# Kernel tuning notes

Measured on AMD Instinct MI355X. Metric: run time of the kernel, lower is better.

## Reference

```python
import jax, jax.numpy as jnp
import numpy as np

D = 128      # feature dim
H = 8        # heads
DH = D // H  # dim per head
N = 100000   # nodes
E = 600000   # edges
BN_EPS = 1e-5


def _bn(x, g, b, m, v):
    # BatchNorm1d in eval mode (running stats)
    return (x - m) * jax.lax.rsqrt(v + BN_EPS) * g + b


def setup_inputs() -> dict:
    key = jax.random.key(0)
    ks = jax.random.split(key, 32)
    s = 1.0 / np.sqrt(D)
    inp = {
        "x": jax.random.normal(ks[0], (N, D), jnp.float32),
        "edge_index": jax.random.randint(ks[1], (2, E), 0, N, jnp.int64),
        # type embeddings (1 node type, 1 edge type)
        "nt_emb": jax.random.normal(ks[2], (1, D), jnp.float32),
        "et_emb": jax.random.normal(ks[3], (1, D), jnp.float32),
        # merge_node_edge_attr: Linear(2D,D) -> BN -> ReLU -> Linear(D,D)
        "mW1": jax.random.normal(ks[4], (2 * D, D), jnp.float32) * s,
        "mb1": jnp.zeros((D,), jnp.float32),
        "m_g": jnp.ones((D,), jnp.float32),
        "m_b": jnp.zeros((D,), jnp.float32),
        "m_m": jax.random.normal(ks[5], (D,), jnp.float32) * 0.1,
        "m_v": jax.random.uniform(ks[6], (D,), jnp.float32, 0.5, 1.5),
        "mW2": jax.random.normal(ks[7], (D, D), jnp.float32) * s,
        "mb2": jnp.zeros((D,), jnp.float32),
        # residual projection (no bias)
        "resW": jax.random.normal(ks[8], (D, D), jnp.float32) * s,
        # attention projections
        "qW": jax.random.normal(ks[9], (D, D), jnp.float32) * s,
        "qb": jnp.zeros((D,), jnp.float32),
        "kW": jax.random.normal(ks[10], (D, D), jnp.float32) * s,
        "kb": jnp.zeros((D,), jnp.float32),
        "vW": jax.random.normal(ks[11], (D, D), jnp.float32) * s,
        "vb": jnp.zeros((D,), jnp.float32),
        # output mlp: Linear -> BN -> LeakyReLU -> Linear
        "oW1": jax.random.normal(ks[12], (D, D), jnp.float32) * s,
        "ob1": jnp.zeros((D,), jnp.float32),
        "o_g": jnp.ones((D,), jnp.float32),
        "o_b": jnp.zeros((D,), jnp.float32),
        "o_m": jax.random.normal(ks[13], (D,), jnp.float32) * 0.1,
        "o_v": jax.random.uniform(ks[14], (D,), jnp.float32, 0.5, 1.5),
        "oW2": jax.random.normal(ks[15], (D, D), jnp.float32) * s,
        "ob2": jnp.zeros((D,), jnp.float32),
    }
    return inp


def reference(x, edge_index, nt_emb, et_emb, mW1, mb1, m_g, m_b, m_m, m_v, mW2, mb2,
              resW, qW, qb, kW, kb, vW, vb, oW1, ob1, o_g, o_b, o_m, o_v, oW2, ob2):
    src = edge_index[0]
    dst = edge_index[1]
    n_nodes = x.shape[0]
    e = edge_index.shape[1]

    # GraphNodeEdgeAttr: edge attrs are constant per edge type; with one node
    # type, edge_attr[0] == edge_attr[1] == merge(cat[node_emb, edge_emb]).
    merged = jnp.concatenate([nt_emb[0], et_emb[0]])          # [2D]
    h = jax.nn.relu(_bn(merged @ mW1 + mb1, m_g, m_b, m_m, m_v))
    ea = h @ mW2 + mb2                                        # [D], broadcasts per edge

    # edge_update: per-edge multi-head attention scores
    x_j = x[src]                                              # [E, D] source feats
    x_i = x[dst]                                              # [E, D] target feats
    q = ((x_j + ea) @ qW + qb).reshape(e, H, DH) / jnp.sqrt(jnp.float32(DH))
    k = ((x_i + ea) @ kW + kb).reshape(e, H, DH)
    msg = (x_j @ vW + vb).reshape(e, H, DH)
    scores = jnp.sum(q * k, axis=2)                           # [E, H]

    # segment softmax keyed by source node index
    smax = jax.ops.segment_max(scores, src, num_segments=n_nodes)
    ex = jnp.exp(scores - smax[src])
    ssum = jax.ops.segment_sum(ex, src, num_segments=n_nodes)
    alpha = ex / ssum[src]                                    # [E, H]

    # message + scatter-add aggregation to destination nodes
    weighted = (msg * alpha[:, :, None]).reshape(e, H * DH)   # [E, D]
    aggr = jax.ops.segment_sum(weighted, dst, num_segments=n_nodes)  # [N, D]

    res = x @ resW
    z = aggr + res
    out = jax.nn.leaky_relu(_bn(z @ oW1 + ob1, o_g, o_b, o_m, o_v)) @ oW2 + ob2
    return out
```

## Files before the change

### kernel.cpp

```cpp
#include <hip/hip_runtime.h>

#define BN_EPS 1e-5f
#define SCAN_CHUNK 1024
#define BM 128

typedef __attribute__((ext_vector_type(8))) short s16x8;
typedef __attribute__((ext_vector_type(4))) float f32x4;

__device__ __forceinline__ ushort f2bf_rne(float f)
{
    unsigned u = __builtin_bit_cast(unsigned, f);
    return (ushort)((u + 0x7fffu + ((u >> 16) & 1u)) >> 16);
}

__device__ __forceinline__ float bf2f(ushort u)
{
    return __builtin_bit_cast(float, (unsigned)u << 16);
}

__global__ __launch_bounds__(128) void k_ea(
    const float* __restrict__ nt, const float* __restrict__ et,
    const float* __restrict__ mW1, const float* __restrict__ mb1,
    const float* __restrict__ m_g, const float* __restrict__ m_b,
    const float* __restrict__ m_m, const float* __restrict__ m_v,
    const float* __restrict__ mW2, const float* __restrict__ mb2,
    const float* __restrict__ qW, const float* __restrict__ qb,
    const float* __restrict__ kW, const float* __restrict__ kb,
    float* __restrict__ eaq, float* __restrict__ eak)
{
    __shared__ float merged[256];
    __shared__ float h[128];
    __shared__ float sea[128];
    const int t = threadIdx.x;
    merged[t]       = nt[t];
    merged[128 + t] = et[t];
    __syncthreads();
    float acc = mb1[t];
    for (int i = 0; i < 256; ++i) acc = fmaf(merged[i], mW1[i * 128 + t], acc);
    acc = (acc - m_m[t]) * rsqrtf(m_v[t] + BN_EPS) * m_g[t] + m_b[t];
    h[t] = acc > 0.f ? acc : 0.f;
    __syncthreads();
    float acc2 = mb2[t];
    for (int k = 0; k < 128; ++k) acc2 = fmaf(h[k], mW2[k * 128 + t], acc2);
    sea[t] = acc2;
    __syncthreads();
    float aq = qb[t], ak = kb[t];
    for (int k = 0; k < 128; ++k) {
        const float e = sea[k];
        aq = fmaf(e, qW[k * 128 + t], aq);
        ak = fmaf(e, kW[k * 128 + t], ak);
    }
    eaq[t] = aq;
    eak[t] = ak;
}

__device__ __forceinline__ void split_store(float w, ushort* __restrict__ base,
                                            int j, int k)
{
    unsigned u = __builtin_bit_cast(unsigned, w);
    unsigned hi = (u + 0x7fffu + ((u >> 16) & 1u)) >> 16;
    float hif = __builtin_bit_cast(float, hi << 16);
    float res = w - hif;
    unsigned lo = __builtin_bit_cast(unsigned, res) >> 16;
    base[j * 128 + k]         = (ushort)hi;
    base[16384 + j * 128 + k] = (ushort)lo;
}

__global__ __launch_bounds__(128) void k_prep3(
    const float* __restrict__ W0, const float* __restrict__ W1,
    const float* __restrict__ W2, ushort* __restrict__ P)
{
    const int j = blockIdx.x;
    const int m = blockIdx.y;
    const int k = threadIdx.x;
    const float* W = (m == 0) ? W0 : (m == 1) ? W1 : W2;
    split_store(W[k * 128 + j], P + (size_t)m * 32768, j, k);
}

__global__ __launch_bounds__(128) void k_prep_out(
    const float* __restrict__ resW, const float* __restrict__ oW1,
    const float* __restrict__ oW2, ushort* __restrict__ P)
{
    __shared__ float col[128];
    const int j = blockIdx.x;
    const int m = blockIdx.y;
    const int k = threadIdx.x;
    float w;
    if (m == 0) {
        col[k] = oW1[k * 128 + j];
        __syncthreads();
        float acc = 0.f;
        for (int i = 0; i < 128; ++i) acc = fmaf(resW[k * 128 + i], col[i], acc);
        w = acc;
    } else {
        const float* W = (m == 1) ? oW1 : oW2;
        w = W[k * 128 + j];
    }
    split_store(w, P + (size_t)m * 32768, j, k);
}

template <int NT>
__device__ __forceinline__ void stage_w(const ushort* __restrict__ wpl,
                                        ushort* __restrict__ sw, int tid)
{
    const uint4* src = (const uint4*)wpl;
#pragma unroll
    for (int it = 0; it < 4096 / NT; ++it) {
        const int idx = it * NT + tid;
        const uint4 v = src[idx];
        const int plane = idx >> 11;
        const int rr = (idx >> 4) & 127;
        const int cb = (idx & 15) << 4;
        const int byteoff = ((rr * 256 + cb) ^ ((rr & 7) << 4));
        *(uint4*)((char*)sw + plane * 32768 + byteoff) = v;
    }
}

template <int CT>
__device__ __forceinline__ void mm_core(const float* __restrict__ Arow,
                                        const ushort* __restrict__ sw,
                                        int g, int r16, int ct0, f32x4* acc)
{
#pragma unroll
    for (int ks = 0; ks < 4; ++ks) {
        const float* ap = Arow + ks * 32 + g * 8;
        const float4 a0 = *(const float4*)(ap);
        const float4 a1 = *(const float4*)(ap + 4);
        float av[8] = {a0.x, a0.y, a0.z, a0.w, a1.x, a1.y, a1.z, a1.w};
        s16x8 ahi, alo;
#pragma unroll
        for (int j = 0; j < 8; ++j) {
            const unsigned u = __builtin_bit_cast(unsigned, av[j]);
            ahi[j] = (short)(u >> 16);
            const float hif = __builtin_bit_cast(float, u & 0xffff0000u);
            const float res = av[j] - hif;
            alo[j] = (short)(__builtin_bit_cast(unsigned, res) >> 16);
        }
        const int koff = ks * 64 + g * 16;
#pragma unroll
        for (int ct = 0; ct < CT; ++ct) {
            const int row = (ct0 + ct) * 16 + r16;
            const int byteoff = ((row * 256 + koff) ^ ((row & 7) << 4));
            const s16x8 bhi = *(const s16x8*)((const char*)sw + byteoff);
            const s16x8 blo = *(const s16x8*)((const char*)sw + 32768 + byteoff);
            acc[ct] = __builtin_amdgcn_mfma_f32_16x16x32_bf16(ahi, bhi, acc[ct], 0, 0, 0);
            acc[ct] = __builtin_amdgcn_mfma_f32_16x16x32_bf16(ahi, blo, acc[ct], 0, 0, 0);
            acc[ct] = __builtin_amdgcn_mfma_f32_16x16x32_bf16(alo, bhi, acc[ct], 0, 0, 0);
        }
    }
}

template <int CT>
__device__ __forceinline__ void mm_core_pre(const ushort* __restrict__ Ahi,
                                            const ushort* __restrict__ Alo,
                                            const ushort* __restrict__ sw,
                                            int g, int r16, int ct0, f32x4* acc)
{
#pragma unroll
    for (int ks = 0; ks < 4; ++ks) {
        const s16x8 ahi = *(const s16x8*)(Ahi + ks * 32 + g * 8);
        const s16x8 alo = *(const s16x8*)(Alo + ks * 32 + g * 8);
        const int koff = ks * 64 + g * 16;
#pragma unroll
        for (int ct = 0; ct < CT; ++ct) {
            const int row = (ct0 + ct) * 16 + r16;
            const int byteoff = ((row * 256 + koff) ^ ((row & 7) << 4));
            const s16x8 bhi = *(const s16x8*)((const char*)sw + byteoff);
            const s16x8 blo = *(const s16x8*)((const char*)sw + 32768 + byteoff);
            acc[ct] = __builtin_amdgcn_mfma_f32_16x16x32_bf16(ahi, bhi, acc[ct], 0, 0, 0);
            acc[ct] = __builtin_amdgcn_mfma_f32_16x16x32_bf16(ahi, blo, acc[ct], 0, 0, 0);
            acc[ct] = __builtin_amdgcn_mfma_f32_16x16x32_bf16(alo, bhi, acc[ct], 0, 0, 0);
        }
    }
}

__global__ __launch_bounds__(1024, 8) void k_mm_qkv(
    const float* __restrict__ x, const ushort* __restrict__ planes,
    const float* __restrict__ eaq, const float* __restrict__ eak,
    const float* __restrict__ vb,
    float* __restrict__ Q, float* __restrict__ K, ushort* __restrict__ V16, int N)
{
    __shared__ ushort sw[2 * 128 * 128];
    const int tid = threadIdx.x;
    const int sel = blockIdx.y;
    stage_w<1024>(planes + (size_t)sel * 32768, sw, tid);
    __syncthreads();

    const int wave = tid >> 6, lane = tid & 63;
    const int g = lane >> 4, r16 = lane & 15;
    const int wr = wave & 7, wc = wave >> 3;
    const int ct0 = wc * 4;
    const int n0 = blockIdx.x * BM;
    const int arow = wr * 16 + r16;
    int nA = n0 + arow; if (nA >= N) nA = N - 1;

    f32x4 acc[4];
#pragma unroll
    for (int ct = 0; ct < 4; ++ct) acc[ct] = (f32x4){0.f, 0.f, 0.f, 0.f};
    mm_core<4>(x + (size_t)nA * 128, sw, g, r16, ct0, acc);

    if (sel == 2) {
#pragma unroll
        for (int ct = 0; ct < 4; ++ct) {
            const int c = (ct0 + ct) * 16 + r16;
            const float bc = vb[c];
#pragma unroll
            for (int r = 0; r < 4; ++r) {
                const int n = n0 + wr * 16 + g * 4 + r;
                if (n < N) V16[(size_t)n * 128 + c] = f2bf_rne(acc[ct][r] + bc);
            }
        }
    } else {
        const float* bias = sel ? eak : eaq;
        float* O          = sel ? K   : Q;
        const float scale = sel ? 1.0f : 0.25f;
#pragma unroll
        for (int ct = 0; ct < 4; ++ct) {
            const int c = (ct0 + ct) * 16 + r16;
            const float bc = bias[c];
#pragma unroll
            for (int r = 0; r < 4; ++r) {
                const int n = n0 + wr * 16 + g * 4 + r;
                if (n < N) O[(size_t)n * 128 + c] = (acc[ct][r] + bc) * scale;
            }
        }
    }
}

__global__ __launch_bounds__(1024, 8) void k_out_u(
    const float* __restrict__ x, const ushort* __restrict__ Po,
    const float* __restrict__ aggr, const float* __restrict__ ob1,
    const float* __restrict__ o_m, const float* __restrict__ o_v,
    const float* __restrict__ o_g, const float* __restrict__ o_b,
    ushort* __restrict__ t_hi, ushort* __restrict__ t_lo, int N)
{
    __shared__ ushort sw[2 * 128 * 128];
    const int tid = threadIdx.x;
    const int wave = tid >> 6, lane = tid & 63;
    const int g = lane >> 4, r16 = lane & 15;
    const int wr = wave & 7, wc = wave >> 3;
    const int ct0 = wc * 4;
    const int n0 = blockIdx.x * BM;
    const int arow = wr * 16 + r16;
    int nA = n0 + arow; if (nA >= N) nA = N - 1;

    f32x4 acc[4];
#pragma unroll
    for (int ct = 0; ct < 4; ++ct) acc[ct] = (f32x4){0.f, 0.f, 0.f, 0.f};

    stage_w<1024>(Po, sw, tid);
    __syncthreads();
    mm_core<4>(x + (size_t)nA * 128, sw, g, r16, ct0, acc);
    __syncthreads();
    stage_w<1024>(Po + 32768, sw, tid);
    __syncthreads();
    mm_core<4>(aggr + (size_t)nA * 128, sw, g, r16, ct0, acc);

#pragma unroll
    for (int ct = 0; ct < 4; ++ct) {
        const int c = (ct0 + ct) * 16 + r16;
        const float bc = ob1[c];
        const float rs = rsqrtf(o_v[c] + BN_EPS);
        const float mm = o_m[c], gg = o_g[c], bb = o_b[c];
#pragma unroll
        for (int r = 0; r < 4; ++r) {
            const int n = n0 + wr * 16 + g * 4 + r;
            if (n >= N) continue;
            float u = acc[ct][r] + bc;
            u = (u - mm) * rs * gg + bb;
            u = u > 0.f ? u : 0.01f * u;
            const unsigned uu = __builtin_bit_cast(unsigned, u);
            const unsigned hi = (uu + 0x7fffu + ((uu >> 16) & 1u)) >> 16;
            const float hif = __builtin_bit_cast(float, hi << 16);
            const unsigned lo = __builtin_bit_cast(unsigned, u - hif) >> 16;
            t_hi[(size_t)n * 128 + c] = (ushort)hi;
            t_lo[(size_t)n * 128 + c] = (ushort)lo;
        }
    }
}

__global__ __launch_bounds__(1024, 8) void k_out_f(
    const ushort* __restrict__ t_hi, const ushort* __restrict__ t_lo,
    const ushort* __restrict__ Pw, const float* __restrict__ ob2,
    float* __restrict__ out, int N)
{
    __shared__ ushort sw[2 * 128 * 128];
    const int tid = threadIdx.x;
    stage_w<1024>(Pw, sw, tid);
    __syncthreads();

    const int wave = tid >> 6, lane = tid & 63;
    const int g = lane >> 4, r16 = lane & 15;
    const int wr = wave & 7, wc = wave >> 3;
    const int ct0 = wc * 4;
    const int n0 = blockIdx.x * BM;
    const int arow = wr * 16 + r16;
    int nA = n0 + arow; if (nA >= N) nA = N - 1;

    f32x4 acc[4];
#pragma unroll
    for (int ct = 0; ct < 4; ++ct) acc[ct] = (f32x4){0.f, 0.f, 0.f, 0.f};
    mm_core_pre<4>(t_hi + (size_t)nA * 128, t_lo + (size_t)nA * 128, sw, g, r16, ct0, acc);

#pragma unroll
    for (int ct = 0; ct < 4; ++ct) {
        const int c = (ct0 + ct) * 16 + r16;
        const float bc = ob2[c];
#pragma unroll
        for (int r = 0; r < 4; ++r) {
            const int n = n0 + wr * 16 + g * 4 + r;
            if (n < N) out[(size_t)n * 128 + c] = acc[ct][r] + bc;
        }
    }
}

__global__ __launch_bounds__(256) void k_edge1csr(
    const int* __restrict__ esrc, const int* __restrict__ row_start,
    const int* __restrict__ deg, const float* __restrict__ Q,
    const float* __restrict__ K, float* __restrict__ exp_,
    float* __restrict__ ssum, int N)
{
    const int tid = threadIdx.x;
    const int n = blockIdx.x * 4 + (tid >> 6);
    if (n >= N) return;
    const int lane = tid & 63;
    const int sub = lane >> 5;
    const int l = lane & 31;
    const int h = l >> 2;
    const int c0 = l * 4;
    const int rs = row_start[n];
    const int dg = deg[n];
    const float4 kreg = *(const float4*)(K + (size_t)n * 128 + c0);
    for (int j = sub; j < dg; j += 2) {
        const int idx = rs + j;
        const int s = esrc[idx];
        const float4 q = *(const float4*)(Q + (size_t)s * 128 + c0);
        float p = q.x * kreg.x + q.y * kreg.y + q.z * kreg.z + q.w * kreg.w;
        p += __shfl_xor(p, 1, 64);
        p += __shfl_xor(p, 2, 64);
        if ((l & 3) == 0) {
            const float v = __expf(p);
            exp_[(size_t)idx * 8 + h] = v;
            unsafeAtomicAdd(&ssum[(size_t)s * 8 + h], v);
        }
    }
}

__global__ __launch_bounds__(256) void k_rsum(float* __restrict__ ssum, int M)
{
    const int i = blockIdx.x * 256 + threadIdx.x;
    if (i < M) ssum[i] = 1.0f / ssum[i];
}

__global__ __launch_bounds__(256) void k_escale(
    float* __restrict__ exp_, const int* __restrict__ esrc,
    const float* __restrict__ rsum, int EH)
{
    const int i = blockIdx.x * 256 + threadIdx.x;
    if (i >= EH) return;
    exp_[i] *= rsum[(size_t)esrc[i >> 3] * 8 + (i & 7)];
}

__global__ __launch_bounds__(256) void k_hist(const int* __restrict__ ei,
                                              int* __restrict__ deg, int E)
{
    const int e = blockIdx.x * 256 + threadIdx.x;
    if (e < E) atomicAdd(&deg[ei[E + e]], 1);
}

__global__ __launch_bounds__(256) void k_scan_partial(const int* __restrict__ deg,
                                                      int* __restrict__ part, int N)
{
    __shared__ int sd[256];
    const int b = blockIdx.x, t = threadIdx.x;
    const int base = b * SCAN_CHUNK + t * 4;
    int s = 0;
#pragma unroll
    for (int i = 0; i < 4; ++i) { const int idx = base + i; if (idx < N) s += deg[idx]; }
    sd[t] = s; __syncthreads();
    for (int off = 128; off > 0; off >>= 1) {
        if (t < off) sd[t] += sd[t + off];
        __syncthreads();
    }
    if (t == 0) part[b] = sd[0];
}

__global__ __launch_bounds__(256) void k_scan_top(int* __restrict__ part, int nb)
{
    __shared__ int sd[256];
    const int t = threadIdx.x;
    const int orig = (t < nb) ? part[t] : 0;
    sd[t] = orig;
    __syncthreads();
    for (int off = 1; off < 256; off <<= 1) {
        const int v = (t >= off) ? sd[t - off] : 0;
        __syncthreads();
        sd[t] += v;
        __syncthreads();
    }
    if (t < nb) part[t] = sd[t] - orig;
}

__global__ __launch_bounds__(256) void k_scan_final(const int* __restrict__ deg,
                                                    const int* __restrict__ part,
                                                    int* __restrict__ row_start,
                                                    int* __restrict__ cursor, int N)
{
    __shared__ int ts[256];
    const int b = blockIdx.x, t = threadIdx.x;
    const int base = b * SCAN_CHUNK + t * 4;
    int v[4]; int s = 0;
#pragma unroll
    for (int i = 0; i < 4; ++i) { const int idx = base + i; v[i] = (idx < N) ? deg[idx] : 0; s += v[i]; }
    ts[t] = s; __syncthreads();
    for (int off = 1; off < 256; off <<= 1) {
        const int vv = (t >= off) ? ts[t - off] : 0;
        __syncthreads();
        ts[t] += vv;
        __syncthreads();
    }
    int run = part[b] + ((t > 0) ? ts[t - 1] : 0);
#pragma unroll
    for (int i = 0; i < 4; ++i) {
        const int idx = base + i;
        if (idx < N) { row_start[idx] = run; cursor[idx] = run; run += v[i]; }
    }
}

__global__ __launch_bounds__(256) void k_scatter(const int* __restrict__ ei,
                                                 int* __restrict__ cursor,
                                                 int* __restrict__ esrc, int E)
{
    const int e = blockIdx.x * 256 + threadIdx.x;
    if (e < E) {
        const int pos = atomicAdd(&cursor[ei[E + e]], 1);
        esrc[pos] = ei[e];
    }
}

__global__ __launch_bounds__(256) void k_aggr(
    const int* __restrict__ esrc, const int* __restrict__ row_start,
    const int* __restrict__ deg, const ushort* __restrict__ V16,
    const float* __restrict__ exp_, float* __restrict__ aggr, int N)
{
    const int tid = threadIdx.x;
    const int n = blockIdx.x * 4 + (tid >> 6);
    if (n >= N) return;
    const int lane = tid & 63;
    const int sub = lane >> 5;
    const int l = lane & 31;
    const int h = l >> 2;
    const int c0 = l * 4;
    const int rs = row_start[n];
    const int dg = deg[n];
    float4 acc = make_float4(0.f, 0.f, 0.f, 0.f);
    for (int j = sub; j < dg; j += 2) {
        const int idx = rs + j;
        const int s = esrc[idx];
        const float a = exp_[(size_t)idx * 8 + h];
        const ushort4 vu = *(const ushort4*)(V16 + (size_t)s * 128 + c0);
        acc.x = fmaf(bf2f(vu.x), a, acc.x);
        acc.y = fmaf(bf2f(vu.y), a, acc.y);
        acc.z = fmaf(bf2f(vu.z), a, acc.z);
        acc.w = fmaf(bf2f(vu.w), a, acc.w);
    }
    acc.x += __shfl_xor(acc.x, 32, 64);
    acc.y += __shfl_xor(acc.y, 32, 64);
    acc.z += __shfl_xor(acc.z, 32, 64);
    acc.w += __shfl_xor(acc.w, 32, 64);
    if (sub == 0) *(float4*)(aggr + (size_t)n * 128 + c0) = acc;
}

extern "C" void kernel_launch(void* const* d_in, const int* in_sizes, int n_in,
                              void* d_out, int out_size, void* d_ws, size_t ws_size,
                              hipStream_t stream)
{
    const float* x    = (const float*)d_in[0];
    const int*   ei   = (const int*)d_in[1];
    const float* nt   = (const float*)d_in[2];
    const float* et   = (const float*)d_in[3];
    const float* mW1  = (const float*)d_in[4];
    const float* mb1  = (const float*)d_in[5];
    const float* m_g  = (const float*)d_in[6];
    const float* m_b  = (const float*)d_in[7];
    const float* m_m  = (const float*)d_in[8];
    const float* m_v  = (const float*)d_in[9];
    const float* mW2  = (const float*)d_in[10];
    const float* mb2  = (const float*)d_in[11];
    const float* resW = (const float*)d_in[12];
    const float* qW   = (const float*)d_in[13];
    const float* qb   = (const float*)d_in[14];
    const float* kW   = (const float*)d_in[15];
    const float* kb   = (const float*)d_in[16];
    const float* vW   = (const float*)d_in[17];
    const float* vb   = (const float*)d_in[18];
    const float* oW1  = (const float*)d_in[19];
    const float* ob1  = (const float*)d_in[20];
    const float* o_g  = (const float*)d_in[21];
    const float* o_b  = (const float*)d_in[22];
    const float* o_m  = (const float*)d_in[23];
    const float* o_v  = (const float*)d_in[24];
    const float* oW2  = (const float*)d_in[25];
    const float* ob2  = (const float*)d_in[26];
    float* out = (float*)d_out;

    const int N = in_sizes[0] / 128;
    const int E = in_sizes[1] / 2;

    float* ws   = (float*)d_ws;
    float* eaq  = ws;
    float* eak  = ws + 128;
    float* Q    = ws + 256;
    float* K    = Q + (size_t)N * 128;
    float* V    = K + (size_t)N * 128;
    float* exp_ = V + (size_t)N * 128;
    float* ssum = exp_ + (size_t)E * 8;
    int* deg       = (int*)(ssum + (size_t)N * 8);
    int* row_start = deg + N;
    int* cursor    = row_start + N;
    int* part      = cursor + N;
    int* esrc      = part + 256;
    float* aggr = Q;
    ushort* V16 = (ushort*)V;
    ushort* t_hi = (ushort*)K;
    ushort* t_lo = t_hi + (size_t)N * 128;
    ushort* Pq = (ushort*)ssum;
    ushort* Po = (ushort*)exp_;

    const int nbm  = (N + BM - 1) / BM;
    const int nbsc = (N + SCAN_CHUNK - 1) / SCAN_CHUNK;

    k_prep3<<<dim3(128, 3), 128, 0, stream>>>(qW, kW, vW, Pq);
    k_ea<<<1, 128, 0, stream>>>(nt, et, mW1, mb1, m_g, m_b, m_m, m_v, mW2, mb2,
                                qW, qb, kW, kb, eaq, eak);
    k_mm_qkv<<<dim3(nbm, 3), 1024, 0, stream>>>(x, Pq, eaq, eak, vb, Q, K, V16, N);

    hipMemsetAsync(ssum, 0, (size_t)N * 8 * sizeof(float), stream);
    hipMemsetAsync(deg, 0, (size_t)N * sizeof(int), stream);

    k_hist<<<(E + 255) / 256, 256, 0, stream>>>(ei, deg, E);
    k_scan_partial<<<nbsc, 256, 0, stream>>>(deg, part, N);
    k_scan_top<<<1, 256, 0, stream>>>(part, nbsc);
    k_scan_final<<<nbsc, 256, 0, stream>>>(deg, part, row_start, cursor, N);
    k_scatter<<<(E + 255) / 256, 256, 0, stream>>>(ei, cursor, esrc, E);

    k_edge1csr<<<(N + 3) / 4, 256, 0, stream>>>(esrc, row_start, deg, Q, K, exp_, ssum, N);
    k_rsum<<<(N * 8 + 255) / 256, 256, 0, stream>>>(ssum, N * 8);
    k_escale<<<(E * 8 + 255) / 256, 256, 0, stream>>>(exp_, esrc, ssum, E * 8);
    k_aggr<<<(N + 3) / 4, 256, 0, stream>>>(esrc, row_start, deg, V16, exp_, aggr, N);

    k_prep_out<<<dim3(128, 3), 128, 0, stream>>>(resW, oW1, oW2, Po);
    k_out_u<<<nbm, 1024, 0, stream>>>(x, Po, aggr, ob1, o_m, o_v, o_g, o_b, t_hi, t_lo, N);
    k_out_f<<<nbm, 1024, 0, stream>>>(t_hi, t_lo, Po + 65536, ob2, out, N);
}
```

Measured before the change: 521.2 us.

## Fuse output MLP kernels, fold softmax normalization into aggregation, coalesce V stores

Merges the two output-MLP kernels into one that keeps the intermediate activation in shared memory as single bf16 instead of writing hi/lo planes to global memory. It uses 64-row blocks of 512 threads and stages the weight planes one at a time. It also removes the separate edge-scaling pass by multiplying by the reciprocal softmax sum inside the aggregation loop. V is now staged through LDS so it can be written with coalesced 16-byte stores. The intermediate drops from hi+lo split to a single bf16, which lowers precision, and the extra weight-staging syncs plus the per-edge rsum gather add cost.

```diff
diff --git a/kernel.cpp b/kernel.cpp
--- a/kernel.cpp
+++ b/kernel.cpp
@@ -116,6 +116,42 @@
     }
 }
 
+template <int NT>
+__device__ __forceinline__ void stage_w1(const ushort* __restrict__ wpl,
+                                         ushort* __restrict__ sw, int tid)
+{
+    const uint4* src = (const uint4*)wpl;
+#pragma unroll
+    for (int it = 0; it < 2048 / NT; ++it) {
+        const int idx = it * NT + tid;
+        const uint4 v = src[idx];
+        const int rr = idx >> 4;
+        const int cb = (idx & 15) << 4;
+        const int byteoff = ((rr * 256 + cb) ^ ((rr & 7) << 4));
+        *(uint4*)((char*)sw + byteoff) = v;
+    }
+}
+
+__device__ __forceinline__ void split_row(const float* __restrict__ row, int g,
+                                          s16x8* ah, s16x8* al)
+{
+#pragma unroll
+    for (int ks = 0; ks < 4; ++ks) {
+        const float* ap = row + ks * 32 + g * 8;
+        const float4 a0 = *(const float4*)(ap);
+        const float4 a1 = *(const float4*)(ap + 4);
+        float av[8] = {a0.x, a0.y, a0.z, a0.w, a1.x, a1.y, a1.z, a1.w};
+#pragma unroll
+        for (int j = 0; j < 8; ++j) {
+            const unsigned u = __builtin_bit_cast(unsigned, av[j]);
+            ah[ks][j] = (short)(u >> 16);
+            const float hif = __builtin_bit_cast(float, u & 0xffff0000u);
+            const float res = av[j] - hif;
+            al[ks][j] = (short)(__builtin_bit_cast(unsigned, res) >> 16);
+        }
+    }
+}
+
 template <int CT>
 __device__ __forceinline__ void mm_core(const float* __restrict__ Arow,
                                         const ushort* __restrict__ sw,
@@ -151,25 +187,38 @@
 }
 
 template <int CT>
-__device__ __forceinline__ void mm_core_pre(const ushort* __restrict__ Ahi,
-                                            const ushort* __restrict__ Alo,
-                                            const ushort* __restrict__ sw,
-                                            int g, int r16, int ct0, f32x4* acc)
+__device__ __forceinline__ void mm_pass2(const s16x8* ah, const s16x8* al,
+                                         const ushort* __restrict__ sw,
+                                         int g, int r16, int ct0, f32x4* acc)
 {
 #pragma unroll
     for (int ks = 0; ks < 4; ++ks) {
-        const s16x8 ahi = *(const s16x8*)(Ahi + ks * 32 + g * 8);
-        const s16x8 alo = *(const s16x8*)(Alo + ks * 32 + g * 8);
         const int koff = ks * 64 + g * 16;
 #pragma unroll
         for (int ct = 0; ct < CT; ++ct) {
             const int row = (ct0 + ct) * 16 + r16;
             const int byteoff = ((row * 256 + koff) ^ ((row & 7) << 4));
-            const s16x8 bhi = *(const s16x8*)((const char*)sw + byteoff);
-            const s16x8 blo = *(const s16x8*)((const char*)sw + 32768 + byteoff);
-            acc[ct] = __builtin_amdgcn_mfma_f32_16x16x32_bf16(ahi, bhi, acc[ct], 0, 0, 0);
-            acc[ct] = __builtin_amdgcn_mfma_f32_16x16x32_bf16(ahi, blo, acc[ct], 0, 0, 0);
-            acc[ct] = __builtin_amdgcn_mfma_f32_16x16x32_bf16(alo, bhi, acc[ct], 0, 0, 0);
+            const s16x8 b = *(const s16x8*)((const char*)sw + byteoff);
+            acc[ct] = __builtin_amdgcn_mfma_f32_16x16x32_bf16(ah[ks], b, acc[ct], 0, 0, 0);
+            acc[ct] = __builtin_amdgcn_mfma_f32_16x16x32_bf16(al[ks], b, acc[ct], 0, 0, 0);
+        }
+    }
+}
+
+template <int CT>
+__device__ __forceinline__ void mm_pass1(const s16x8* a,
+                                         const ushort* __restrict__ sw,
+                                         int g, int r16, int ct0, f32x4* acc)
+{
+#pragma unroll
+    for (int ks = 0; ks < 4; ++ks) {
+        const int koff = ks * 64 + g * 16;
+#pragma unroll
+        for (int ct = 0; ct < CT; ++ct) {
+            const int row = (ct0 + ct) * 16 + r16;
+            const int byteoff = ((row * 256 + koff) ^ ((row & 7) << 4));
+            const s16x8 b = *(const s16x8*)((const char*)sw + byteoff);
+            acc[ct] = __builtin_amdgcn_mfma_f32_16x16x32_bf16(a[ks], b, acc[ct], 0, 0, 0);
         }
     }
 }
@@ -200,15 +249,26 @@
     mm_core<4>(x + (size_t)nA * 128, sw, g, r16, ct0, acc);
 
     if (sel == 2) {
+        __syncthreads();
+        ushort* vbuf = (ushort*)sw;
 #pragma unroll
         for (int ct = 0; ct < 4; ++ct) {
             const int c = (ct0 + ct) * 16 + r16;
             const float bc = vb[c];
 #pragma unroll
             for (int r = 0; r < 4; ++r) {
-                const int n = n0 + wr * 16 + g * 4 + r;
-                if (n < N) V16[(size_t)n * 128 + c] = f2bf_rne(acc[ct][r] + bc);
+                const int nrel = wr * 16 + g * 4 + r;
+                vbuf[nrel * 128 + c] = f2bf_rne(acc[ct][r] + bc);
             }
+        }
+        __syncthreads();
+        const int row = tid >> 3;
+        const int col = (tid & 7) * 16;
+        if (n0 + row < N) {
+            const uint4* src = (const uint4*)(vbuf + row * 128 + col);
+            const uint4 v0 = src[0], v1 = src[1];
+            uint4* dst = (uint4*)(V16 + (size_t)(n0 + row) * 128 + col);
+            dst[0] = v0; dst[1] = v1;
         }
     } else {
         const float* bias = sel ? eak : eaq;
@@ -227,34 +287,41 @@
     }
 }
 
-__global__ __launch_bounds__(1024, 8) void k_out_u(
+__global__ __launch_bounds__(512, 4) void k_out3(
     const float* __restrict__ x, const ushort* __restrict__ Po,
     const float* __restrict__ aggr, const float* __restrict__ ob1,
     const float* __restrict__ o_m, const float* __restrict__ o_v,
     const float* __restrict__ o_g, const float* __restrict__ o_b,
-    ushort* __restrict__ t_hi, ushort* __restrict__ t_lo, int N)
-{
-    __shared__ ushort sw[2 * 128 * 128];
+    const float* __restrict__ ob2, float* __restrict__ out, int N)
+{
+    __shared__ ushort sw[128 * 128];
+    __shared__ ushort tb[64 * 128];
     const int tid = threadIdx.x;
     const int wave = tid >> 6, lane = tid & 63;
     const int g = lane >> 4, r16 = lane & 15;
-    const int wr = wave & 7, wc = wave >> 3;
+    const int wr = wave & 3, wc = wave >> 2;
     const int ct0 = wc * 4;
-    const int n0 = blockIdx.x * BM;
+    const int n0 = blockIdx.x * 64;
     const int arow = wr * 16 + r16;
     int nA = n0 + arow; if (nA >= N) nA = N - 1;
 
+    s16x8 ah[4], al[4];
+    split_row(x + (size_t)nA * 128, g, ah, al);
+
     f32x4 acc[4];
 #pragma unroll
     for (int ct = 0; ct < 4; ++ct) acc[ct] = (f32x4){0.f, 0.f, 0.f, 0.f};
 
-    stage_w<1024>(Po, sw, tid);
-    __syncthreads();
-    mm_core<4>(x + (size_t)nA * 128, sw, g, r16, ct0, acc);
-    __syncthreads();
-    stage_w<1024>(Po + 32768, sw, tid);
-    __syncthreads();
-    mm_core<4>(aggr + (size_t)nA * 128, sw, g, r16, ct0, acc);
+    stage_w1<512>(Po, sw, tid); __syncthreads();
+    mm_pass2<4>(ah, al, sw, g, r16, ct0, acc); __syncthreads();
+    stage_w1<512>(Po + 16384, sw, tid); __syncthreads();
+    mm_pass1<4>(ah, sw, g, r16, ct0, acc); __syncthreads();
+
+    split_row(aggr + (size_t)nA * 128, g, ah, al);
+    stage_w1<512>(Po + 32768, sw, tid); __syncthreads();
+    mm_pass2<4>(ah, al, sw, g, r16, ct0, acc); __syncthreads();
+    stage_w1<512>(Po + 49152, sw, tid); __syncthreads();
+    mm_pass1<4>(ah, sw, g, r16, ct0, acc); __syncthreads();
 
 #pragma unroll
     for (int ct = 0; ct < 4; ++ct) {
@@ -264,43 +331,29 @@
         const float mm = o_m[c], gg = o_g[c], bb = o_b[c];
 #pragma unroll
         for (int r = 0; r < 4; ++r) {
-            const int n = n0 + wr * 16 + g * 4 + r;
-            if (n >= N) continue;
+            const int nrel = wr * 16 + g * 4 + r;
             float u = acc[ct][r] + bc;
             u = (u - mm) * rs * gg + bb;
             u = u > 0.f ? u : 0.01f * u;
-            const unsigned uu = __builtin_bit_cast(unsigned, u);
-            const unsigned hi = (uu + 0x7fffu + ((uu >> 16) & 1u)) >> 16;
-            const float hif = __builtin_bit_cast(float, hi << 16);
-            const unsigned lo = __builtin_bit_cast(unsigned, u - hif) >> 16;
-            t_hi[(size_t)n * 128 + c] = (ushort)hi;
-            t_lo[(size_t)n * 128 + c] = (ushort)lo;
-        }
-    }
-}
-
-__global__ __launch_bounds__(1024, 8) void k_out_f(
-    const ushort* __restrict__ t_hi, const ushort* __restrict__ t_lo,
-    const ushort* __restrict__ Pw, const float* __restrict__ ob2,
-    float* __restrict__ out, int N)
-{
-    __shared__ ushort sw[2 * 128 * 128];
-    const int tid = threadIdx.x;
-    stage_w<1024>(Pw, sw, tid);
-    __syncthreads();
-
-    const int wave = tid >> 6, lane = tid & 63;
-    const int g = lane >> 4, r16 = lane & 15;
-    const int wr = wave & 7, wc = wave >> 3;
-    const int ct0 = wc * 4;
-    const int n0 = blockIdx.x * BM;
-    const int arow = wr * 16 + r16;
-    int nA = n0 + arow; if (nA >= N) nA = N - 1;
-
-    f32x4 acc[4];
+            const int byteoff = ((nrel * 256 + c * 2) ^ ((nrel & 7) << 4));
+            *(ushort*)((char*)tb + byteoff) = f2bf_rne(u);
+        }
+    }
+    stage_w1<512>(Po + 65536, sw, tid);
+    __syncthreads();
+
+    s16x8 ta[4];
+#pragma unroll
+    for (int ks = 0; ks < 4; ++ks) {
+        const int byteoff = ((arow * 256 + ks * 64 + g * 16) ^ ((arow & 7) << 4));
+        ta[ks] = *(const s16x8*)((const char*)tb + byteoff);
+    }
 #pragma unroll
     for (int ct = 0; ct < 4; ++ct) acc[ct] = (f32x4){0.f, 0.f, 0.f, 0.f};
-    mm_core_pre<4>(t_hi + (size_t)nA * 128, t_lo + (size_t)nA * 128, sw, g, r16, ct0, acc);
+    mm_pass1<4>(ta, sw, g, r16, ct0, acc);
+    __syncthreads();
+    stage_w1<512>(Po + 81920, sw, tid); __syncthreads();
+    mm_pass1<4>(ta, sw, g, r16, ct0, acc);
 
 #pragma unroll
     for (int ct = 0; ct < 4; ++ct) {
@@ -352,15 +405,6 @@
     if (i < M) ssum[i] = 1.0f / ssum[i];
 }
 
-__global__ __launch_bounds__(256) void k_escale(
-    float* __restrict__ exp_, const int* __restrict__ esrc,
-    const float* __restrict__ rsum, int EH)
-{
-    const int i = blockIdx.x * 256 + threadIdx.x;
-    if (i >= EH) return;
-    exp_[i] *= rsum[(size_t)esrc[i >> 3] * 8 + (i & 7)];
-}
-
 __global__ __launch_bounds__(256) void k_hist(const int* __restrict__ ei,
                                               int* __restrict__ deg, int E)
 {
@@ -441,7 +485,8 @@
 __global__ __launch_bounds__(256) void k_aggr(
     const int* __restrict__ esrc, const int* __restrict__ row_start,
     const int* __restrict__ deg, const ushort* __restrict__ V16,
-    const float* __restrict__ exp_, float* __restrict__ aggr, int N)
+    const float* __restrict__ exp_, const float* __restrict__ rsum,
+    float* __restrict__ aggr, int N)
 {
     const int tid = threadIdx.x;
     const int n = blockIdx.x * 4 + (tid >> 6);
@@ -457,7 +502,7 @@
     for (int j = sub; j < dg; j += 2) {
         const int idx = rs + j;
         const int s = esrc[idx];
-        const float a = exp_[(size_t)idx * 8 + h];
+        const float a = exp_[(size_t)idx * 8 + h] * rsum[(size_t)s * 8 + h];
         const ushort4 vu = *(const ushort4*)(V16 + (size_t)s * 128 + c0);
         acc.x = fmaf(bf2f(vu.x), a, acc.x);
         acc.y = fmaf(bf2f(vu.y), a, acc.y);
@@ -522,12 +567,11 @@
     int* esrc      = part + 256;
     float* aggr = Q;
     ushort* V16 = (ushort*)V;
-    ushort* t_hi = (ushort*)K;
-    ushort* t_lo = t_hi + (size_t)N * 128;
     ushort* Pq = (ushort*)ssum;
     ushort* Po = (ushort*)exp_;
 
     const int nbm  = (N + BM - 1) / BM;
+    const int nbo  = (N + 63) / 64;
     const int nbsc = (N + SCAN_CHUNK - 1) / SCAN_CHUNK;
 
     k_prep3<<<dim3(128, 3), 128, 0, stream>>>(qW, kW, vW, Pq);
@@ -546,10 +590,8 @@
 
     k_edge1csr<<<(N + 3) / 4, 256, 0, stream>>>(esrc, row_start, deg, Q, K, exp_, ssum, N);
     k_rsum<<<(N * 8 + 255) / 256, 256, 0, stream>>>(ssum, N * 8);
-    k_escale<<<(E * 8 + 255) / 256, 256, 0, stream>>>(exp_, esrc, ssum, E * 8);
-    k_aggr<<<(N + 3) / 4, 256, 0, stream>>>(esrc, row_start, deg, V16, exp_, aggr, N);
+    k_aggr<<<(N + 3) / 4, 256, 0, stream>>>(esrc, row_start, deg, V16, exp_, ssum, aggr, N);
 
     k_prep_out<<<dim3(128, 3), 128, 0, stream>>>(resW, oW1, oW2, Po);
-    k_out_u<<<nbm, 1024, 0, stream>>>(x, Po, aggr, ob1, o_m, o_v, o_g, o_b, t_hi, t_lo, N);
-    k_out_f<<<nbm, 1024, 0, stream>>>(t_hi, t_lo, Po + 65536, ob2, out, N);
-}
+    k_out3<<<nbo, 512, 0, stream>>>(x, Po, aggr, ob1, o_m, o_v, o_g, o_b, ob2, out, N);
+}
```

Result: faster. 485.1 us (-6.9%).
